# Kernel tuning notes

Hardware: AMD Instinct MI355X
Metric: run time of the kernel (lower is better)

The kernel has to match this reference:

```python
import jax, jax.numpy as jnp
import numpy as np

B, N, E, S, A, P, T = 512, 65536, 131072, 256, 512, 2, 64


def setup_inputs() -> dict:
    key = jax.random.key(0)
    ks = jax.random.split(key, 40)
    f32 = jnp.float32

    def g(i, shape, s=0.05):
        return jax.random.normal(ks[i], shape, f32) * s

    inp = {
        'nodes': jax.random.normal(ks[0], (N, S), f32),
        'edge_features': jax.random.normal(ks[1], (E, S), f32),
        'edge_source': jax.random.randint(ks[2], (E,), 0, N),
        'edge_dest': jax.random.randint(ks[3], (E,), 0, N),
        'node_owner': jax.random.randint(ks[4], (N,), 0, B),
        'running': jnp.ones((B,), bool),
        'ref_types': jax.random.randint(ks[5], (B,), 0, T),
        # decision aggregator (transform + sigmoid gate)
        'dec_t_W': g(6, (A, S)), 'dec_t_b': g(7, (A,)),
        'dec_g_W': g(8, (A, S)), 'dec_g_b': jnp.ones((A,), f32),
        # init aggregator
        'init_t_W': g(9, (A, S)), 'init_t_b': g(10, (A,)),
        'init_g_W': g(11, (A, S)), 'init_g_b': jnp.ones((A,), f32),
        # node type decision head + embedding
        'ntd_W': g(12, (T + 1, A)), 'ntd_b': g(13, (T + 1,)),
        'nte': g(14, (T, S), 1.0),
        # f_init
        'f1_W': g(15, (S, S)), 'f1_b': g(16, (S,)),
        'f2_W': g(17, (S, A)),
        # propagator params, stacked over P steps (message_size = 2S)
        'mn_W': g(18, (P, 2 * S, S)),
        'mf_W': g(19, (P, 2 * S, S)),
        'ml2_W': g(20, (P, 2 * S, 2 * S)), 'ml2_b': g(21, (P, 2 * S)),
        'gru_Wih': g(22, (P, 3 * S, 2 * S)), 'gru_Whh': g(23, (P, 3 * S, S)),
        'gru_bih': jnp.zeros((P, 3 * S), f32),
        'gru_bhh': jnp.concatenate(
            [jnp.ones((P, S), f32), jnp.zeros((P, 2 * S), f32)], axis=-1),
    }
    return inp


def _aggregate(nodes, fmask, tW, tb, gW, gb):
    # Aggregator.forward: sigmoid gate * linear transform, pooled per graph
    # via dense 0/1 owner-mask matmul (dropout=0 -> identity).
    gates = jax.nn.sigmoid(nodes @ gW.T + gb)
    data = nodes @ tW.T + tb
    return fmask @ (data * gates)  # [B, A]


def reference(nodes, edge_features, edge_source, edge_dest, node_owner,
              running, ref_types,
              dec_t_W, dec_t_b, dec_g_W, dec_g_b,
              init_t_W, init_t_b, init_g_W, init_g_b,
              ntd_W, ntd_b, nte, f1_W, f1_b, f2_W,
              mn_W, mf_W, ml2_W, ml2_b, gru_Wih, gru_Whh, gru_bih, gru_bhh):
    f32 = nodes.dtype
    fmask = (node_owner[None, :] == jnp.arange(B)[:, None]).astype(f32)  # [B,N]
    # Propagator._node_update_mask: owner_masks[running].sum(0) > 0
    upd = (fmask * running[:, None].astype(f32)).sum(0) > 0  # [N]

    for p in range(P):
        ef = edge_features @ mf_W[p].T                 # [E, 2S]
        nf = nodes @ mn_W[p].T                         # [N, 2S]
        msgs = nf[edge_source] + nf[edge_dest] + ef
        msgs = jnp.tanh(msgs) @ ml2_W[p].T + ml2_b[p]  # message_layer_2
        inputs = jnp.zeros((N, 2 * S), f32)
        inputs = inputs.at[edge_dest].add(msgs).at[edge_source].add(msgs)
        # torch GRUCell (gate order r, z, n)
        gi = inputs @ gru_Wih[p].T + gru_bih[p]
        gh = nodes @ gru_Whh[p].T + gru_bhh[p]
        ir, iz, inn = jnp.split(gi, 3, axis=-1)
        hr, hz, hn = jnp.split(gh, 3, axis=-1)
        r = jax.nn.sigmoid(ir + hr)
        z = jax.nn.sigmoid(iz + hz)
        n = jnp.tanh(inn + r * hn)
        new_nodes = (1.0 - z) * n + z * nodes
        nodes = jnp.where(upd[:, None], new_nodes, nodes)

    # node-type decision
    agg = _aggregate(nodes, fmask, dec_t_W, dec_t_b, dec_g_W, dec_g_b)
    logits = agg @ ntd_W.T + ntd_b                      # [B, T+1]

    # training path: remap_pad (no pad chars present) -> ref + 1
    sel = ref_types + 1                                  # in [1, T]
    logp = jax.nn.log_softmax(logits, axis=-1)
    per_ex = -logp[jnp.arange(B), sel]
    loss = jnp.where(running, per_ex, 0.0).mean()

    # new node features for running graphs
    emb = nte[sel - 1]                                   # [B, S]
    init_feats = _aggregate(nodes, fmask, init_t_W, init_t_b,
                            init_g_W, init_g_b)
    new_features = emb @ f1_W.T + f1_b + init_feats @ f2_W.T  # [B, S]
    return logits, new_features, loss
```

## Files before the change

### kernel.cpp

```cpp
#include <hip/hip_runtime.h>
#include <hip/hip_bf16.h>
#include <math.h>

#define BG 512
#define NN 65536
#define EE 131072
#define SD 256
#define AD 512
#define PP 2
#define TD 64

typedef __attribute__((ext_vector_type(8))) short sx8;
typedef __attribute__((ext_vector_type(4))) short sx4;
typedef __attribute__((ext_vector_type(4))) float fx4;

__device__ __forceinline__ float bs2f(short s) {
    union { unsigned u; float f; } x; x.u = ((unsigned)(unsigned short)s) << 16; return x.f;
}
__device__ __forceinline__ short f2bs(float f) {
    union { float f; unsigned u; } x; x.f = f;
    unsigned r = x.u + 0x7fffu + ((x.u >> 16) & 1u);
    return (short)(r >> 16);
}
__device__ __forceinline__ float fast_tanh(float x) {
    float xc = fminf(fmaxf(x, -15.f), 15.f);
    float e = __expf(2.f * xc);
    return __fdividef(e - 1.f, e + 1.f);
}
__device__ __forceinline__ float fast_sigm(float x) {
    float xc = fminf(fmaxf(x, -30.f), 30.f);
    float e = __expf(-xc);
    return __fdividef(1.f, 1.f + e);
}
__device__ __forceinline__ bool run_flag(const void* runv, int idx) {
    const unsigned char* r8 = (const unsigned char*)runv;
    const int* r32 = (const int*)runv;
    return (r8[idx] != 0) || (r32[idx] != 0);
}

__device__ __forceinline__ void gload16(const short* g, short* l) {
    __builtin_amdgcn_global_load_lds(
        (const __attribute__((address_space(1))) void*)g,
        (__attribute__((address_space(3))) void*)l, 16, 0, 0);
}

template<int EPI>
__launch_bounds__(256, 3)
__global__ void gemm_bt(const short* __restrict__ Abp, const short* __restrict__ Wp,
                        const float* __restrict__ bias, const float* __restrict__ bias2,
                        short* __restrict__ Cout, float* __restrict__ Fout,
                        float* __restrict__ FoutB,
                        const float* __restrict__ biasB, const float* __restrict__ biasB2,
                        const short* __restrict__ nfp,
                        const int* __restrict__ esrc, const int* __restrict__ edst,
                        int K, int NC, int NT, int nsplit)
{
    __shared__ __align__(16) short sA[3 * 4096];
    __shared__ __align__(16) short sB[3 * 4096];
    const int t = threadIdx.x;
    const int lane = t & 63;
    const int w = t >> 6;

    const int nwg = gridDim.x;
    const int q = nwg >> 3;
    const int wg = (blockIdx.x & 7) * q + (blockIdx.x >> 3);
    const int mt = wg / NT;
    const int nt = wg - mt * NT;
    const int m0 = mt * 128;
    const int n0 = nt * 128;

    const int wm = (w >> 1) * 64;
    const int wn = (w & 1) * 64;
    const int lr = lane & 15;
    const int lg = lane >> 4;

    fx4 acc[4][4];
#pragma unroll
    for (int i = 0; i < 4; i++)
#pragma unroll
        for (int j = 0; j < 4; j++) { fx4 z = {0.f, 0.f, 0.f, 0.f}; acc[i][j] = z; }

    const int r = t >> 2;
    const int cblk = (t & 3) ^ ((r >> 1) & 3);
    const short* gA = Abp + (size_t)(m0 + r) * K + cblk * 8;
    const short* gB = Wp + (size_t)(n0 + r) * K + cblk * 8;
    const size_t rowskip = (size_t)64 * K;

    auto STAGE = [&](int b, int kk) {
        gload16(gA + kk,           sA + b * 4096 + w * 512);
        gload16(gA + kk + rowskip, sA + b * 4096 + 2048 + w * 512);
        gload16(gB + kk,           sB + b * 4096 + w * 512);
        gload16(gB + kk + rowskip, sB + b * 4096 + 2048 + w * 512);
    };

    STAGE(0, 0);
    STAGE(1, 32);

    int es[4], ed[4];
    if (EPI == 2) {
#pragma unroll
        for (int mi = 0; mi < 4; mi++) {
            const int m = m0 + wm + mi * 16 + lr;
            es[mi] = esrc[m]; ed[mi] = edst[m];
        }
    }

    const int T = K >> 5;
    int cur = 0;
    const int xa = (lr >> 1) & 3;
    for (int i = 0; i < T; i++) {
        __builtin_amdgcn_s_barrier();
        if (i + 2 < T) {
            STAGE((cur >= 1) ? cur - 1 : cur + 2, (i + 2) << 5);
            asm volatile("s_waitcnt vmcnt(8)" ::: "memory");
        } else if (i + 1 < T) {
            asm volatile("s_waitcnt vmcnt(4)" ::: "memory");
        } else {
            asm volatile("s_waitcnt vmcnt(0)" ::: "memory");
        }
        __builtin_amdgcn_s_barrier();
        const short* cA = sA + cur * 4096;
        const short* cB = sB + cur * 4096;
        sx8 af[4], bfr[4];
#pragma unroll
        for (int mi = 0; mi < 4; mi++)
            af[mi] = *(const sx8*)(cA + (wm + mi * 16 + lr) * 32 + (lg ^ xa) * 8);
#pragma unroll
        for (int ni = 0; ni < 4; ni++)
            bfr[ni] = *(const sx8*)(cB + (wn + ni * 16 + lr) * 32 + (lg ^ xa) * 8);
#pragma unroll
        for (int mi = 0; mi < 4; mi++)
#pragma unroll
            for (int ni = 0; ni < 4; ni++) {
                if (EPI == 4)
                    acc[mi][ni] = __builtin_amdgcn_mfma_f32_16x16x32_bf16(
                        af[mi], bfr[ni], acc[mi][ni], 0, 0, 0);
                else
                    acc[mi][ni] = __builtin_amdgcn_mfma_f32_16x16x32_bf16(
                        bfr[ni], af[mi], acc[mi][ni], 0, 0, 0);
            }
        cur = (cur == 2) ? 0 : cur + 1;
    }

    if (EPI == 4) {
        const bool useB = (n0 >= nsplit);
        float* fo = useB ? FoutB : Fout;
        const float* tb = useB ? biasB : bias;
        const float* gb = useB ? biasB2 : bias2;
        const int ln0 = useB ? (n0 - nsplit) : n0;
#pragma unroll
        for (int mi = 0; mi < 4; mi++) {
#pragma unroll
            for (int rg = 0; rg < 4; rg++) {
                const int m = m0 + wm + mi * 16 + lg * 4 + rg;
#pragma unroll
                for (int ni = 0; ni < 4; ni += 2) {
                    const int rc = (((ln0 + wn + ni * 16) >> 5) << 4) + lr;
                    float dv = acc[mi][ni][rg] + tb[rc];
                    float gv = fast_sigm(acc[mi][ni + 1][rg] + gb[rc]);
                    fo[(size_t)m * 512 + rc] = dv * gv;
                }
            }
        }
    } else {
#pragma unroll
        for (int mi = 0; mi < 4; mi++) {
            const int m = m0 + wm + mi * 16 + lr;
            if (EPI == 2) {
                const short* ps = nfp + (size_t)es[mi] * NC + n0;
                const short* pd = nfp + (size_t)ed[mi] * NC + n0;
                short* co = Cout + (size_t)m * NC + n0;
#pragma unroll
                for (int ni = 0; ni < 4; ni++) {
                    const int nc = wn + ni * 16 + lg * 4;
                    sx4 a4 = *(const sx4*)(ps + nc);
                    sx4 b4 = *(const sx4*)(pd + nc);
                    sx4 o;
#pragma unroll
                    for (int rg = 0; rg < 4; rg++)
                        o[rg] = f2bs(fast_tanh(acc[mi][ni][rg]
                                               + bs2f(a4[rg]) + bs2f(b4[rg])));
                    *(sx4*)(co + nc) = o;
                }
            } else {
                short* co = Cout + (size_t)m * NC + n0;
#pragma unroll
                for (int ni = 0; ni < 4; ni++) {
                    const int nc = wn + ni * 16 + lg * 4;
                    fx4 vb = {0.f, 0.f, 0.f, 0.f};
                    if (bias) vb = *(const fx4*)(bias + n0 + nc);
                    sx4 o;
#pragma unroll
                    for (int rg = 0; rg < 4; rg++)
                        o[rg] = f2bs(acc[mi][ni][rg] + vb[rg]);
                    *(sx4*)(co + nc) = o;
                }
            }
        }
    }
}

__global__ void k_castw(const float* __restrict__ in, short* __restrict__ out)
{
    size_t i = ((size_t)blockIdx.x * 256 + threadIdx.x) * 4;
    fx4 v = *(const fx4*)(in + i);
    sx4 o;
#pragma unroll
    for (int u = 0; u < 4; u++) o[u] = f2bs(v[u]);
    *(sx4*)(out + i) = o;
}

__global__ void k_cast_pair(const float* __restrict__ tW, const float* __restrict__ gW,
                            short* __restrict__ out)
{
    size_t i = ((size_t)blockIdx.x * 256 + threadIdx.x) * 4;
    const int r2 = (int)(i >> 8);
    const int c = (int)(i & 255);
    const int src = ((r2 >> 5) << 4) | (r2 & 15);
    const float* W = ((r2 >> 4) & 1) ? gW : tW;
    fx4 v = *(const fx4*)(W + (size_t)src * 256 + c);
    sx4 o;
#pragma unroll
    for (int u = 0; u < 4; u++) o[u] = f2bs(v[u]);
    *(sx4*)(out + i) = o;
}

__global__ void k_count2(const int* __restrict__ a, const int* __restrict__ b,
                         int* __restrict__ deg, int n)
{
    int i = blockIdx.x * 256 + threadIdx.x;
    if (i < n) { atomicAdd(&deg[a[i]], 1); atomicAdd(&deg[b[i]], 1); }
}
__global__ void k_count1(const int* __restrict__ a, int* __restrict__ deg, int n)
{
    int i = blockIdx.x * 256 + threadIdx.x;
    if (i < n) atomicAdd(&deg[a[i]], 1);
}
__global__ void k_scan(const int* __restrict__ deg, int* __restrict__ offs, int n)
{
    __shared__ int part[256];
    const int t = threadIdx.x;
    const int chunk = n >> 8;
    const int base = t * chunk;
    int s = 0;
    for (int i = 0; i < chunk; i++) s += deg[base + i];
    part[t] = s;
    __syncthreads();
    for (int off = 1; off < 256; off <<= 1) {
        int v = (t >= off) ? part[t - off] : 0;
        __syncthreads();
        part[t] += v;
        __syncthreads();
    }
    int run = (t > 0) ? part[t - 1] : 0;
    for (int i = 0; i < chunk; i++) {
        offs[base + i] = run;
        run += deg[base + i];
    }
    if (t == 255) offs[n] = part[255];
}
__global__ void k_fill2(const int* __restrict__ a, const int* __restrict__ b,
                        const int* __restrict__ offs, int* __restrict__ cur,
                        int* __restrict__ elist, int n)
{
    int i = blockIdx.x * 256 + threadIdx.x;
    if (i < n) {
        int p = atomicAdd(&cur[a[i]], 1); elist[offs[a[i]] + p] = i;
        int q = atomicAdd(&cur[b[i]], 1); elist[offs[b[i]] + q] = i;
    }
}
__global__ void k_fill1(const int* __restrict__ own, const int* __restrict__ offs,
                        int* __restrict__ cur, int* __restrict__ nlist, int n)
{
    int i = blockIdx.x * 256 + threadIdx.x;
    if (i < n) {
        int p = atomicAdd(&cur[own[i]], 1); nlist[offs[own[i]] + p] = i;
    }
}

__global__ void k_edge_gather(const short* __restrict__ msgs, const int* __restrict__ offs,
                              const int* __restrict__ elist, short* __restrict__ inp)
{
    const int node = blockIdx.x * 4 + (threadIdx.x >> 6);
    const int c = (threadIdx.x & 63) * 8;
    const int s0 = offs[node], s1 = offs[node + 1];
    float acc[8] = {0.f, 0.f, 0.f, 0.f, 0.f, 0.f, 0.f, 0.f};
    for (int s = s0; s < s1; s++) {
        const int e = elist[s];
        sx8 v = *(const sx8*)(msgs + (size_t)e * 512 + c);
#pragma unroll
        for (int u = 0; u < 8; u++) acc[u] += bs2f(v[u]);
    }
    sx8 o;
#pragma unroll
    for (int u = 0; u < 8; u++) o[u] = f2bs(acc[u]);
    *(sx8*)(inp + (size_t)node * 512 + c) = o;
}

__global__ void k_owner_reduce(const float* __restrict__ gp, const int* __restrict__ offsB,
                               const int* __restrict__ nlist, float* __restrict__ agg)
{
    const int b = blockIdx.x, t = threadIdx.x;
    const int s0 = offsB[b], s1 = offsB[b + 1];
    float a0 = 0.f, a1 = 0.f;
    for (int s = s0; s < s1; s++) {
        const int n = nlist[s];
        float2 v = *(const float2*)(gp + (size_t)n * 512 + t * 2);
        a0 += v.x; a1 += v.y;
    }
    agg[(size_t)b * 512 + t * 2] = a0;
    agg[(size_t)b * 512 + t * 2 + 1] = a1;
}

__global__ void k_gru(const short* __restrict__ gi, const short* __restrict__ gh,
                      short* __restrict__ nodes,
                      const int* __restrict__ owner, const void* __restrict__ runv)
{
    const int n = blockIdx.x * 4 + (threadIdx.x >> 6);
    const int t = threadIdx.x & 63;
    const bool run = run_flag(runv, owner[n]);
    const size_t gb = (size_t)n * 768 + t * 4;
    sx4 vir = *(const sx4*)(gi + gb);
    sx4 viz = *(const sx4*)(gi + gb + 256);
    sx4 vin = *(const sx4*)(gi + gb + 512);
    sx4 whr = *(const sx4*)(gh + gb);
    sx4 whz = *(const sx4*)(gh + gb + 256);
    sx4 whn = *(const sx4*)(gh + gb + 512);
    const size_t nbase = (size_t)n * 256 + t * 4;
    sx4 old4 = *(const sx4*)(nodes + nbase);
    sx4 outb;
#pragma unroll
    for (int u = 0; u < 4; u++) {
        float old = bs2f(old4[u]);
        float rr = fast_sigm(bs2f(vir[u]) + bs2f(whr[u]));
        float zz = fast_sigm(bs2f(viz[u]) + bs2f(whz[u]));
        float nn = fast_tanh(bs2f(vin[u]) + rr * bs2f(whn[u]));
        float nv = (1.f - zz) * nn + zz * old;
        outb[u] = run ? f2bs(nv) : old4[u];
    }
    *(sx4*)(nodes + nbase) = outb;
}

__global__ void k_logits(const float* __restrict__ agg, const float* __restrict__ Wt,
                         const float* __restrict__ bt, float* __restrict__ logitsF,
                         float* __restrict__ outL)
{
    __shared__ float row[512];
    const int b = blockIdx.x, t = threadIdx.x;
    for (int k = t; k < 512; k += 128) row[k] = agg[(size_t)b * 512 + k];
    __syncthreads();
    if (t < TD + 1) {
        float acc = bt[t];
        const float* wr = Wt + (size_t)t * 512;
        for (int k = 0; k < 512; k++) acc += row[k] * wr[k];
        logitsF[b * (TD + 1) + t] = acc;
        outL[b * (TD + 1) + t] = acc;
    }
}

__global__ void k_loss(const float* __restrict__ logitsF, const int* __restrict__ reft,
                       const void* __restrict__ runv, float* __restrict__ outLoss)
{
    __shared__ float red[512];
    const int b = threadIdx.x;
    const float* lr = logitsF + b * (TD + 1);
    float mx = lr[0];
    for (int k = 1; k < TD + 1; k++) mx = fmaxf(mx, lr[k]);
    float se = 0.f;
    for (int k = 0; k < TD + 1; k++) se += expf(lr[k] - mx);
    const int sel = reft[b] + 1;
    float pe = logf(se) + mx - lr[sel];
    red[b] = run_flag(runv, b) ? pe : 0.f;
    __syncthreads();
    for (int s = 256; s > 0; s >>= 1) {
        if (b < s) red[b] += red[b + s];
        __syncthreads();
    }
    if (b == 0) outLoss[0] = red[0] / (float)BG;
}

__global__ void k_newfeat(const float* __restrict__ aggi, const float* __restrict__ nte,
                          const int* __restrict__ reft, const float* __restrict__ f1W,
                          const float* __restrict__ f1b, const float* __restrict__ f2W,
                          float* __restrict__ outNF)
{
    __shared__ float emb[256];
    __shared__ float ag[512];
    const int b = blockIdx.x, t = threadIdx.x;
    const int rt = reft[b];
    emb[t] = nte[(size_t)rt * 256 + t];
    ag[t] = aggi[(size_t)b * 512 + t];
    ag[t + 256] = aggi[(size_t)b * 512 + 256 + t];
    __syncthreads();
    float acc = f1b[t];
    const float* w1 = f1W + (size_t)t * 256;
    for (int k = 0; k < 256; k++) acc += emb[k] * w1[k];
    const float* w2 = f2W + (size_t)t * 512;
    for (int a = 0; a < 512; a++) acc += ag[a] * w2[a];
    outNF[(size_t)b * 256 + t] = acc;
}

extern "C" void kernel_launch(void* const* d_in, const int* in_sizes, int n_in,
                              void* d_out, int out_size, void* d_ws, size_t ws_size,
                              hipStream_t stream)
{
    (void)in_sizes; (void)n_in; (void)out_size;
    const float* in_nodes = (const float*)d_in[0];
    const float* in_ef    = (const float*)d_in[1];
    const int*   e_src    = (const int*)d_in[2];
    const int*   e_dst    = (const int*)d_in[3];
    const int*   owner    = (const int*)d_in[4];
    const void*  running  = d_in[5];
    const int*   reft     = (const int*)d_in[6];
    const float* dec_tW = (const float*)d_in[7];
    const float* dec_tb = (const float*)d_in[8];
    const float* dec_gW = (const float*)d_in[9];
    const float* dec_gb = (const float*)d_in[10];
    const float* init_tW = (const float*)d_in[11];
    const float* init_tb = (const float*)d_in[12];
    const float* init_gW = (const float*)d_in[13];
    const float* init_gb = (const float*)d_in[14];
    const float* ntdW = (const float*)d_in[15];
    const float* ntdb = (const float*)d_in[16];
    const float* nte  = (const float*)d_in[17];
    const float* f1W  = (const float*)d_in[18];
    const float* f1b  = (const float*)d_in[19];
    const float* f2W  = (const float*)d_in[20];
    const float* mnW  = (const float*)d_in[21];
    const float* mfW  = (const float*)d_in[22];
    const float* ml2W = (const float*)d_in[23];
    const float* ml2b = (const float*)d_in[24];
    const float* Wih  = (const float*)d_in[25];
    const float* Whh  = (const float*)d_in[26];
    const float* bih  = (const float*)d_in[27];
    const float* bhh  = (const float*)d_in[28];

    float* outL    = (float*)d_out;
    float* outNF   = outL + BG * (TD + 1);
    float* outLoss = outNF + BG * SD;

    size_t off = 0;
    auto take = [&](size_t bytes) -> void* {
        void* p = (char*)d_ws + off;
        off += (bytes + 255) & ~(size_t)255;
        return p;
    };
    short* nodes_bf  = (short*)take((size_t)NN * SD * 2);
    short* ef_bf     = (short*)take((size_t)EE * SD * 2);
    short* bufC      = (short*)take((size_t)NN * 512 * 2);
    short* bufD      = (short*)take((size_t)EE * 512 * 2);
    short* bufM      = (short*)take((size_t)EE * 512 * 2);
    short* bufI      = (short*)take((size_t)NN * 512 * 2);
    float* aggD      = (float*)take((size_t)BG * AD * 4);
    float* aggI      = (float*)take((size_t)BG * AD * 4);
    float* logitsF   = (float*)take((size_t)BG * (TD + 1) * 4);
    short* mnWb  = (short*)take((size_t)PP * 512 * 256 * 2);
    short* mfWb  = (short*)take((size_t)PP * 512 * 256 * 2);
    short* ml2Wb = (short*)take((size_t)PP * 512 * 512 * 2);
    short* WihB  = (short*)take((size_t)PP * 768 * 512 * 2);
    short* WhhB  = (short*)take((size_t)PP * 768 * 256 * 2);
    short* W4agg = (short*)take((size_t)2048 * 256 * 2);
    int* deg_e = (int*)take((size_t)NN * 4);
    int* offs_e = (int*)take((size_t)(NN + 1) * 4);
    int* cur_e = (int*)take((size_t)NN * 4);
    int* elist = (int*)take((size_t)2 * EE * 4);
    int* degB = (int*)take((size_t)BG * 4);
    int* offsB = (int*)take((size_t)(BG + 1) * 4);
    int* curB = (int*)take((size_t)BG * 4);
    int* nlist = (int*)take((size_t)NN * 4);
    if (off > ws_size) return;

    short* gi = bufD;
    short* gh = bufM;
    float* gpD = (float*)bufM;
    float* gpI = (float*)bufD;

    k_castw<<<NN * SD / 1024, 256, 0, stream>>>(in_nodes, nodes_bf);
    k_castw<<<EE * SD / 1024, 256, 0, stream>>>(in_ef, ef_bf);
    k_castw<<<PP * 512 * 256 / 1024, 256, 0, stream>>>(mnW, mnWb);
    k_castw<<<PP * 512 * 256 / 1024, 256, 0, stream>>>(mfW, mfWb);
    k_castw<<<PP * 512 * 512 / 1024, 256, 0, stream>>>(ml2W, ml2Wb);
    k_castw<<<PP * 768 * 512 / 1024, 256, 0, stream>>>(Wih, WihB);
    k_castw<<<PP * 768 * 256 / 1024, 256, 0, stream>>>(Whh, WhhB);
    k_cast_pair<<<1024 * 256 / 1024, 256, 0, stream>>>(dec_tW, dec_gW, W4agg);
    k_cast_pair<<<1024 * 256 / 1024, 256, 0, stream>>>(init_tW, init_gW,
                                                       W4agg + 1024 * 256);

    hipMemsetAsync(deg_e, 0, (size_t)NN * 4, stream);
    hipMemsetAsync(cur_e, 0, (size_t)NN * 4, stream);
    hipMemsetAsync(degB, 0, (size_t)BG * 4, stream);
    hipMemsetAsync(curB, 0, (size_t)BG * 4, stream);
    k_count2<<<(EE + 255) / 256, 256, 0, stream>>>(e_src, e_dst, deg_e, EE);
    k_scan<<<1, 256, 0, stream>>>(deg_e, offs_e, NN);
    k_fill2<<<(EE + 255) / 256, 256, 0, stream>>>(e_src, e_dst, offs_e, cur_e, elist, EE);
    k_count1<<<(NN + 255) / 256, 256, 0, stream>>>(owner, degB, NN);
    k_scan<<<1, 256, 0, stream>>>(degB, offsB, BG);
    k_fill1<<<(NN + 255) / 256, 256, 0, stream>>>(owner, offsB, curB, nlist, NN);

    for (int p = 0; p < PP; p++) {
        gemm_bt<0><<<NN / 128 * 4, 256, 0, stream>>>(
            nodes_bf, mnWb + (size_t)p * 512 * 256, nullptr, nullptr, bufC,
            nullptr, nullptr, nullptr, nullptr, nullptr, nullptr, nullptr,
            256, 512, 4, 0);
        gemm_bt<2><<<EE / 128 * 4, 256, 0, stream>>>(
            ef_bf, mfWb + (size_t)p * 512 * 256, nullptr, nullptr, bufD,
            nullptr, nullptr, nullptr, nullptr, bufC, e_src, e_dst,
            256, 512, 4, 0);
        gemm_bt<0><<<EE / 128 * 4, 256, 0, stream>>>(
            bufD, ml2Wb + (size_t)p * 512 * 512, ml2b + (size_t)p * 512, nullptr,
            bufM, nullptr, nullptr, nullptr, nullptr, nullptr, nullptr, nullptr,
            512, 512, 4, 0);
        k_edge_gather<<<NN / 4, 256, 0, stream>>>(bufM, offs_e, elist, bufI);
        gemm_bt<0><<<NN / 128 * 6, 256, 0, stream>>>(
            bufI, WihB + (size_t)p * 768 * 512, bih + (size_t)p * 768, nullptr,
            gi, nullptr, nullptr, nullptr, nullptr, nullptr, nullptr, nullptr,
            512, 768, 6, 0);
        gemm_bt<0><<<NN / 128 * 6, 256, 0, stream>>>(
            nodes_bf, WhhB + (size_t)p * 768 * 256, bhh + (size_t)p * 768, nullptr,
            gh, nullptr, nullptr, nullptr, nullptr, nullptr, nullptr, nullptr,
            256, 768, 6, 0);
        k_gru<<<NN / 4, 256, 0, stream>>>(gi, gh, nodes_bf, owner, running);
    }

    gemm_bt<4><<<NN / 128 * 16, 256, 0, stream>>>(
        nodes_bf, W4agg, dec_tb, dec_gb, nullptr, gpD, gpI,
        init_tb, init_gb, nullptr, nullptr, nullptr,
        256, 2048, 16, 1024);
    k_owner_reduce<<<BG, 256, 0, stream>>>(gpD, offsB, nlist, aggD);
    k_owner_reduce<<<BG, 256, 0, stream>>>(gpI, offsB, nlist, aggI);

    k_logits<<<BG, 128, 0, stream>>>(aggD, ntdW, ntdb, logitsF, outL);
    k_loss<<<1, 512, 0, stream>>>(logitsF, reft, running, outLoss);
    k_newfeat<<<BG, 256, 0, stream>>>(aggI, nte, reft, f1W, f1b, f2W, outNF);
}
```

Baseline: 1.983 ms.

## Use double-buffered GEMM with higher occupancy and bf16 aggregator outputs

Replaces the three-stage LDS pipeline in the bf16 GEMM with a two-buffer loop synchronised by __syncthreads, which cuts shared memory per block, and raises the launch-bounds occupancy target from 3 to 5 blocks. The gated aggregator epilogue now writes bf16 instead of fp32, and the owner reduction reads bf16. This halves the intermediate traffic for the aggregator path. The risks are less latency hiding with only one prefetch stage in flight, register pressure from the tighter occupancy bound, and extra rounding in the pooled sums.

```diff
diff --git a/kernel.cpp b/kernel.cpp
--- a/kernel.cpp
+++ b/kernel.cpp
@@ -45,18 +45,18 @@
 }
 
 template<int EPI>
-__launch_bounds__(256, 3)
+__launch_bounds__(256, 5)
 __global__ void gemm_bt(const short* __restrict__ Abp, const short* __restrict__ Wp,
                         const float* __restrict__ bias, const float* __restrict__ bias2,
-                        short* __restrict__ Cout, float* __restrict__ Fout,
-                        float* __restrict__ FoutB,
+                        short* __restrict__ Cout, short* __restrict__ Fout,
+                        short* __restrict__ FoutB,
                         const float* __restrict__ biasB, const float* __restrict__ biasB2,
                         const short* __restrict__ nfp,
                         const int* __restrict__ esrc, const int* __restrict__ edst,
                         int K, int NC, int NT, int nsplit)
 {
-    __shared__ __align__(16) short sA[3 * 4096];
-    __shared__ __align__(16) short sB[3 * 4096];
+    __shared__ __align__(16) short sA[2 * 4096];
+    __shared__ __align__(16) short sB[2 * 4096];
     const int t = threadIdx.x;
     const int lane = t & 63;
     const int w = t >> 6;
@@ -94,7 +94,6 @@
     };
 
     STAGE(0, 0);
-    STAGE(1, 32);
 
     int es[4], ed[4];
     if (EPI == 2) {
@@ -105,22 +104,13 @@
         }
     }
 
-    const int T = K >> 5;
-    int cur = 0;
+    __syncthreads();
+    int buf = 0;
     const int xa = (lr >> 1) & 3;
-    for (int i = 0; i < T; i++) {
-        __builtin_amdgcn_s_barrier();
-        if (i + 2 < T) {
-            STAGE((cur >= 1) ? cur - 1 : cur + 2, (i + 2) << 5);
-            asm volatile("s_waitcnt vmcnt(8)" ::: "memory");
-        } else if (i + 1 < T) {
-            asm volatile("s_waitcnt vmcnt(4)" ::: "memory");
-        } else {
-            asm volatile("s_waitcnt vmcnt(0)" ::: "memory");
-        }
-        __builtin_amdgcn_s_barrier();
-        const short* cA = sA + cur * 4096;
-        const short* cB = sB + cur * 4096;
+    for (int kk = 0; kk < K; kk += 32) {
+        if (kk + 32 < K) STAGE(buf ^ 1, kk + 32);
+        const short* cA = sA + buf * 4096;
+        const short* cB = sB + buf * 4096;
         sx8 af[4], bfr[4];
 #pragma unroll
         for (int mi = 0; mi < 4; mi++)
@@ -139,12 +129,13 @@
                     acc[mi][ni] = __builtin_amdgcn_mfma_f32_16x16x32_bf16(
                         bfr[ni], af[mi], acc[mi][ni], 0, 0, 0);
             }
-        cur = (cur == 2) ? 0 : cur + 1;
+        __syncthreads();
+        buf ^= 1;
     }
 
     if (EPI == 4) {
         const bool useB = (n0 >= nsplit);
-        float* fo = useB ? FoutB : Fout;
+        short* fo = useB ? FoutB : Fout;
         const float* tb = useB ? biasB : bias;
         const float* gb = useB ? biasB2 : bias2;
         const int ln0 = useB ? (n0 - nsplit) : n0;
@@ -158,7 +149,7 @@
                     const int rc = (((ln0 + wn + ni * 16) >> 5) << 4) + lr;
                     float dv = acc[mi][ni][rg] + tb[rc];
                     float gv = fast_sigm(acc[mi][ni + 1][rg] + gb[rc]);
-                    fo[(size_t)m * 512 + rc] = dv * gv;
+                    fo[(size_t)m * 512 + rc] = f2bs(dv * gv);
                 }
             }
         }
@@ -297,7 +288,7 @@
     *(sx8*)(inp + (size_t)node * 512 + c) = o;
 }
 
-__global__ void k_owner_reduce(const float* __restrict__ gp, const int* __restrict__ offsB,
+__global__ void k_owner_reduce(const short* __restrict__ gp, const int* __restrict__ offsB,
                                const int* __restrict__ nlist, float* __restrict__ agg)
 {
     const int b = blockIdx.x, t = threadIdx.x;
@@ -305,8 +296,8 @@
     float a0 = 0.f, a1 = 0.f;
     for (int s = s0; s < s1; s++) {
         const int n = nlist[s];
-        float2 v = *(const float2*)(gp + (size_t)n * 512 + t * 2);
-        a0 += v.x; a1 += v.y;
+        const short* pp = gp + (size_t)n * 512 + t * 2;
+        a0 += bs2f(pp[0]); a1 += bs2f(pp[1]);
     }
     agg[(size_t)b * 512 + t * 2] = a0;
     agg[(size_t)b * 512 + t * 2 + 1] = a1;
@@ -472,8 +463,8 @@
 
     short* gi = bufD;
     short* gh = bufM;
-    float* gpD = (float*)bufM;
-    float* gpI = (float*)bufD;
+    short* gpD = bufM;
+    short* gpI = bufD;
 
     k_castw<<<NN * SD / 1024, 256, 0, stream>>>(in_nodes, nodes_bf);
     k_castw<<<EE * SD / 1024, 256, 0, stream>>>(in_ef, ef_bf);
```

Result: slower. 2.362 ms (+19.1%).
